# Optimization experiments

Measured on AMD Instinct MI355X. Metric: run time of the kernel, lower is better.

The kernel has to match this reference:

```python
import jax, jax.numpy as jnp
import numpy as np

N = 200000
H = W = 1024
C_IN, C_MID = 256, 64
EPS = 1e-6


def _build_neighbor_idx():
    # Sample N unique occupied sites on an HxW grid; build 3x3 kernel maps.
    rng = np.random.default_rng(0)
    perm = rng.permutation(H * W)[:N]
    grid = -np.ones(H * W, dtype=np.int64)
    grid[perm] = np.arange(N)
    ys, xs = perm // W, perm % W
    maps = []
    for dy in (-1, 0, 1):
        for dx in (-1, 0, 1):
            ny, nx = ys + dy, xs + dx
            valid = (ny >= 0) & (ny < H) & (nx >= 0) & (nx < W)
            lin = np.clip(ny * W + nx, 0, H * W - 1)
            nb = grid[lin]
            maps.append(np.where(valid & (nb >= 0), nb, N))  # sentinel N = missing
    return jnp.asarray(np.stack(maps).astype(np.int32))  # [9, N]


def setup_inputs() -> dict:
    key = jax.random.key(0)
    ks = jax.random.split(key, 4)
    return {
        "x": jax.random.normal(ks[0], (N, C_IN), jnp.float32),
        "W1": jax.random.normal(ks[1], (C_IN, C_MID), jnp.float32) * (C_IN ** -0.5),
        "W2": jax.random.normal(ks[2], (9, C_MID, C_MID), jnp.float32) * ((9 * C_MID) ** -0.5),
        "W3": jax.random.normal(ks[3], (C_MID, C_IN), jnp.float32) * (C_MID ** -0.5),
        "g1": jnp.ones((C_MID,), jnp.float32),
        "b1": jnp.zeros((C_MID,), jnp.float32),
        "g2": jnp.ones((C_MID,), jnp.float32),
        "b2": jnp.zeros((C_MID,), jnp.float32),
        "g3": jnp.ones((C_IN,), jnp.float32),
        "b3": jnp.zeros((C_IN,), jnp.float32),
        "neighbor_idx": _build_neighbor_idx(),
    }


def _ln(h, g, b):
    mu = jnp.mean(h, axis=-1, keepdims=True)
    var = jnp.mean(jnp.square(h - mu), axis=-1, keepdims=True)
    return (h - mu) * jax.lax.rsqrt(var + EPS) * g + b


def reference(x, W1, W2, W3, g1, b1, g2, b2, g3, b3, neighbor_idx):
    # conv1 (1x1 sparse conv == per-point linear) -> LN -> GELU
    h = jax.nn.gelu(_ln(x @ W1, g1, b1), approximate=False)
    # conv2: 3x3 sparse conv via gather-GEMM over kernel maps, sentinel row = zeros
    h_pad = jnp.concatenate([h, jnp.zeros((1, h.shape[1]), h.dtype)], axis=0)
    gathered = h_pad[neighbor_idx]               # [9, N, C_MID]
    h = jnp.einsum('knc,kcd->nd', gathered, W2)  # [N, C_MID]
    h = jax.nn.gelu(_ln(h, g2, b2), approximate=False)
    # conv3 (1x1) -> LN, residual, GELU
    h = _ln(h @ W3, g3, b3)
    return jax.nn.gelu(h + x, approximate=False)
```

## Files before the change

kernel.cpp:

```cpp
#include <hip/hip_runtime.h>
#include <math.h>

#define NPTS 200000
#define LNEPS 1e-6f

typedef unsigned short u16;
typedef __attribute__((ext_vector_type(4))) float  f4;
typedef __attribute__((ext_vector_type(8))) short  s8;

__device__ __forceinline__ u16 f2b(float f) {
    union { float f; unsigned u; } v; v.f = f;
    unsigned r = v.u + 0x7fffu + ((v.u >> 16) & 1u);
    return (u16)(r >> 16);
}

__device__ __forceinline__ float gelu_f(float v) {
    float u = v * (0.7978845608028654f + 0.035677408136300125f * v * v);
    u = fminf(u, 15.0f);
    float e = __builtin_amdgcn_exp2f(u * 2.8853900817779268f);
    return 0.5f * v * (1.0f + (e - 1.0f) * __builtin_amdgcn_rcpf(e + 1.0f));
}

__global__ __launch_bounds__(256) void k0_convw(
    const float* __restrict__ W1, const float* __restrict__ W2,
    const float* __restrict__ W3,
    u16* __restrict__ W1f, u16* __restrict__ W2f, u16* __restrict__ W3f,
    u16* __restrict__ h1)
{
    int t = blockIdx.x * 256 + threadIdx.x;
    if (t < 16384) {
        int j = t & 7, l = (t >> 3) & 63, ks = (t >> 9) & 7, nt = t >> 12;
        int k = 32 * ks + (l >> 4) * 8 + j;
        int n = 16 * nt + (l & 15);
        W1f[t] = f2b(W1[k * 64 + n]);
    }
    if (t < 36864) {
        int kk = t >> 12;
        int r = t & 4095;
        int j = r & 7, l = (r >> 3) & 63, ks = (r >> 9) & 1, nt = r >> 10;
        int k = 32 * ks + (l >> 4) * 8 + j;
        int n = 16 * nt + (l & 15);
        W2f[t] = f2b(W2[(kk * 64 + k) * 64 + n]);
    }
    if (t < 16384) {
        int j = t & 7, l = (t >> 3) & 63, ks = (t >> 9) & 1, nt = t >> 10;
        int k = 32 * ks + (l >> 4) * 8 + j;
        int n = 16 * nt + (l & 15);
        W3f[t] = f2b(W3[k * 256 + n]);
    }
    if (t < 64) h1[(long)NPTS * 64 + t] = 0;
}

__global__ __launch_bounds__(256) void k1_conv1(
    const float* __restrict__ x, const u16* __restrict__ W1f,
    const float* __restrict__ g1, const float* __restrict__ b1,
    u16* __restrict__ h1)
{
    int tid = threadIdx.x;
    int w = tid >> 6, l = tid & 63, lg = l >> 4, lr = l & 15;
    long base = (long)blockIdx.x * 64 + w * 16;
    const float* xrow = x + (base + lr) * 256;

    f4 xa[16];
    #pragma unroll
    for (int ks = 0; ks < 8; ++ks) {
        xa[2 * ks]     = *(const f4*)(xrow + 32 * ks + lg * 8);
        xa[2 * ks + 1] = *(const f4*)(xrow + 32 * ks + lg * 8 + 4);
    }

    f4 acc[4] = {};
    #pragma unroll
    for (int ks = 0; ks < 8; ++ks) {
        f4 a0 = xa[2 * ks], a1 = xa[2 * ks + 1];
        s8 a;
        a[0] = (short)f2b(a0[0]); a[1] = (short)f2b(a0[1]);
        a[2] = (short)f2b(a0[2]); a[3] = (short)f2b(a0[3]);
        a[4] = (short)f2b(a1[0]); a[5] = (short)f2b(a1[1]);
        a[6] = (short)f2b(a1[2]); a[7] = (short)f2b(a1[3]);
        #pragma unroll
        for (int nt = 0; nt < 4; ++nt) {
            s8 b = *(const s8*)(W1f + ((nt * 8 + ks) * 64 + l) * 8);
            acc[nt] = __builtin_amdgcn_mfma_f32_16x16x32_bf16(a, b, acc[nt], 0, 0, 0);
        }
    }

    #pragma unroll
    for (int r = 0; r < 4; ++r) {
        float sv = 0.f, qv = 0.f;
        #pragma unroll
        for (int nt = 0; nt < 4; ++nt) { float v = acc[nt][r]; sv += v; qv += v * v; }
        #pragma unroll
        for (int m = 1; m < 16; m <<= 1) { sv += __shfl_xor(sv, m); qv += __shfl_xor(qv, m); }
        float mu  = sv * (1.0f / 64.0f);
        float var = qv * (1.0f / 64.0f) - mu * mu;
        float rs  = rsqrtf(var + LNEPS);
        long row = base + lg * 4 + r;
        #pragma unroll
        for (int nt = 0; nt < 4; ++nt) {
            int col = 16 * nt + lr;
            float v = (acc[nt][r] - mu) * rs * g1[col] + b1[col];
            h1[row * 64 + col] = f2b(gelu_f(v));
        }
    }
}

__global__ __launch_bounds__(256, 4) void k2a_conv2(
    const u16* __restrict__ h1, const u16* __restrict__ W2f,
    const float* __restrict__ g2, const float* __restrict__ b2,
    const int* __restrict__ nidx, u16* __restrict__ h2)
{
    int tid = threadIdx.x;
    int w = tid >> 6, l = tid & 63, lg = l >> 4, lr = l & 15;
    long base = (long)blockIdx.x * 64 + w * 16;
    long rowa = base + lr;

    int idxs[9];
    #pragma unroll
    for (int k = 0; k < 9; ++k) idxs[k] = nidx[(long)k * NPTS + rowa];

    s8 afr[9][2];
    #pragma unroll
    for (int k = 0; k < 9; ++k) {
        const u16* arow = h1 + (long)idxs[k] * 64;
        afr[k][0] = *(const s8*)(arow + lg * 8);
        afr[k][1] = *(const s8*)(arow + 32 + lg * 8);
    }

    f4 acc2[4] = {};
    #pragma unroll
    for (int k = 0; k < 9; ++k) {
        #pragma unroll
        for (int ks = 0; ks < 2; ++ks) {
            #pragma unroll
            for (int nt = 0; nt < 4; ++nt) {
                s8 b = *(const s8*)(W2f + (long)k * 4096 + ((nt * 2 + ks) * 64 + l) * 8);
                acc2[nt] = __builtin_amdgcn_mfma_f32_16x16x32_bf16(afr[k][ks], b, acc2[nt], 0, 0, 0);
            }
        }
    }

    #pragma unroll
    for (int r = 0; r < 4; ++r) {
        float sv = 0.f, qv = 0.f;
        #pragma unroll
        for (int nt = 0; nt < 4; ++nt) { float v = acc2[nt][r]; sv += v; qv += v * v; }
        #pragma unroll
        for (int m = 1; m < 16; m <<= 1) { sv += __shfl_xor(sv, m); qv += __shfl_xor(qv, m); }
        float mu  = sv * (1.0f / 64.0f);
        float var = qv * (1.0f / 64.0f) - mu * mu;
        float rs  = rsqrtf(var + LNEPS);
        long row = base + lg * 4 + r;
        #pragma unroll
        for (int nt = 0; nt < 4; ++nt) {
            int col = 16 * nt + lr;
            float v = (acc2[nt][r] - mu) * rs * g2[col] + b2[col];
            h2[row * 64 + col] = f2b(gelu_f(v));
        }
    }
}

__global__ __launch_bounds__(256, 4) void k2b_conv3(
    const u16* __restrict__ h2, const u16* __restrict__ W3f,
    const float* __restrict__ x,
    const float* __restrict__ g3, const float* __restrict__ b3,
    float* __restrict__ out)
{
    int tid = threadIdx.x;
    int w = tid >> 6, l = tid & 63, lg = l >> 4, lr = l & 15;
    long base = (long)blockIdx.x * 64 + w * 16;

    const u16* arow = h2 + (base + lr) * 64;
    s8 a0 = *(const s8*)(arow + lg * 8);
    s8 a1 = *(const s8*)(arow + 32 + lg * 8);

    f4 acc3[16] = {};
    #pragma unroll
    for (int nt = 0; nt < 16; ++nt) {
        s8 b0 = *(const s8*)(W3f + ((nt * 2 + 0) * 64 + l) * 8);
        s8 b1 = *(const s8*)(W3f + ((nt * 2 + 1) * 64 + l) * 8);
        acc3[nt] = __builtin_amdgcn_mfma_f32_16x16x32_bf16(a0, b0, acc3[nt], 0, 0, 0);
        acc3[nt] = __builtin_amdgcn_mfma_f32_16x16x32_bf16(a1, b1, acc3[nt], 0, 0, 0);
    }

    #pragma unroll
    for (int r = 0; r < 4; ++r) {
        float sv = 0.f, qv = 0.f;
        #pragma unroll
        for (int nt = 0; nt < 16; ++nt) { float v = acc3[nt][r]; sv += v; qv += v * v; }
        #pragma unroll
        for (int m = 1; m < 16; m <<= 1) { sv += __shfl_xor(sv, m); qv += __shfl_xor(qv, m); }
        float mu  = sv * (1.0f / 256.0f);
        float var = qv * (1.0f / 256.0f) - mu * mu;
        float rs  = rsqrtf(var + LNEPS);
        long row = base + lg * 4 + r;
        const float* xr = x + row * 256;
        float* outr = out + row * 256;
        #pragma unroll
        for (int nt = 0; nt < 16; ++nt) {
            int col = 16 * nt + lr;
            float v = (acc3[nt][r] - mu) * rs * g3[col] + b3[col];
            v += xr[col];
            outr[col] = gelu_f(v);
        }
    }
}

extern "C" void kernel_launch(void* const* d_in, const int* in_sizes, int n_in,
                              void* d_out, int out_size, void* d_ws, size_t ws_size,
                              hipStream_t stream)
{
    const float* x  = (const float*)d_in[0];
    const float* W1 = (const float*)d_in[1];
    const float* W2 = (const float*)d_in[2];
    const float* W3 = (const float*)d_in[3];
    const float* g1 = (const float*)d_in[4];
    const float* b1 = (const float*)d_in[5];
    const float* g2 = (const float*)d_in[6];
    const float* b2 = (const float*)d_in[7];
    const float* g3 = (const float*)d_in[8];
    const float* b3 = (const float*)d_in[9];
    const int* nidx = (const int*)d_in[10];
    float* out = (float*)d_out;

    char* ws = (char*)d_ws;
    u16* W1f = (u16*)(ws);
    u16* W2f = (u16*)(ws + 32768);
    u16* W3f = (u16*)(ws + 106496);
    u16* h1  = (u16*)(ws + 139264);
    u16* h2  = (u16*)(ws + 139264 + 25600128);

    hipLaunchKernelGGL(k0_convw, dim3(144), dim3(256), 0, stream,
                       W1, W2, W3, W1f, W2f, W3f, h1);
    hipLaunchKernelGGL(k1_conv1, dim3(3125), dim3(256), 0, stream,
                       x, W1f, g1, b1, h1);
    hipLaunchKernelGGL(k2a_conv2, dim3(3125), dim3(256), 0, stream,
                       h1, W2f, g2, b2, nidx, h2);
    hipLaunchKernelGGL(k2b_conv3, dim3(3125), dim3(256), 0, stream,
                       h2, W3f, x, g3, b3, out);
}
```

Baseline: 220.2 us.

## Stage conv1 input and conv3 epilogue through LDS for coalesced access

conv1 now loads the fp32 x tile cooperatively with coalesced 16-byte loads, converts it to bf16 once and stores it in a swizzled LDS tile. The MFMA A-fragments are then read from LDS. conv3 writes the normalized outputs to an LDS staging buffer so the residual read of x and the output store become row-contiguous float4 accesses instead of scattered scalar ones. This adds LDS usage and block barriers, and lowers the occupancy hint for conv3.

```diff
diff --git a/kernel.cpp b/kernel.cpp
--- a/kernel.cpp
+++ b/kernel.cpp
@@ -7,6 +7,7 @@
 typedef unsigned short u16;
 typedef __attribute__((ext_vector_type(4))) float  f4;
 typedef __attribute__((ext_vector_type(8))) short  s8;
+typedef __attribute__((ext_vector_type(4))) short  s4;
 
 __device__ __forceinline__ u16 f2b(float f) {
     union { float f; unsigned u; } v; v.f = f;
@@ -56,27 +57,32 @@
     const float* __restrict__ g1, const float* __restrict__ b1,
     u16* __restrict__ h1)
 {
+    __shared__ __align__(16) u16 xt[64][256];
     int tid = threadIdx.x;
+    long base = (long)blockIdx.x * 64;
+
+    #pragma unroll
+    for (int p = 0; p < 16; ++p) {
+        int row  = p * 4 + (tid >> 6);
+        int col4 = (tid & 63) * 4;
+        f4 v = *(const f4*)(x + (base + row) * 256 + col4);
+        s4 bv;
+        bv[0] = (short)f2b(v[0]); bv[1] = (short)f2b(v[1]);
+        bv[2] = (short)f2b(v[2]); bv[3] = (short)f2b(v[3]);
+        int byte = (col4 * 2) ^ ((row & 7) << 4);
+        *(s4*)((char*)&xt[row][0] + byte) = bv;
+    }
+    __syncthreads();
+
     int w = tid >> 6, l = tid & 63, lg = l >> 4, lr = l & 15;
-    long base = (long)blockIdx.x * 64 + w * 16;
-    const float* xrow = x + (base + lr) * 256;
-
-    f4 xa[16];
+    int arow = w * 16 + lr;
+    long mbase = base + w * 16;
+
+    f4 acc[4] = {};
     #pragma unroll
     for (int ks = 0; ks < 8; ++ks) {
-        xa[2 * ks]     = *(const f4*)(xrow + 32 * ks + lg * 8);
-        xa[2 * ks + 1] = *(const f4*)(xrow + 32 * ks + lg * 8 + 4);
-    }
-
-    f4 acc[4] = {};
-    #pragma unroll
-    for (int ks = 0; ks < 8; ++ks) {
-        f4 a0 = xa[2 * ks], a1 = xa[2 * ks + 1];
-        s8 a;
-        a[0] = (short)f2b(a0[0]); a[1] = (short)f2b(a0[1]);
-        a[2] = (short)f2b(a0[2]); a[3] = (short)f2b(a0[3]);
-        a[4] = (short)f2b(a1[0]); a[5] = (short)f2b(a1[1]);
-        a[6] = (short)f2b(a1[2]); a[7] = (short)f2b(a1[3]);
+        int byte = ((ks * 64 + lg * 16)) ^ ((arow & 7) << 4);
+        s8 a = *(const s8*)((const char*)&xt[arow][0] + byte);
         #pragma unroll
         for (int nt = 0; nt < 4; ++nt) {
             s8 b = *(const s8*)(W1f + ((nt * 8 + ks) * 64 + l) * 8);
@@ -94,7 +100,7 @@
         float mu  = sv * (1.0f / 64.0f);
         float var = qv * (1.0f / 64.0f) - mu * mu;
         float rs  = rsqrtf(var + LNEPS);
-        long row = base + lg * 4 + r;
+        long row = mbase + lg * 4 + r;
         #pragma unroll
         for (int nt = 0; nt < 4; ++nt) {
             int col = 16 * nt + lr;
@@ -159,12 +165,13 @@
     }
 }
 
-__global__ __launch_bounds__(256, 4) void k2b_conv3(
+__global__ __launch_bounds__(256, 3) void k2b_conv3(
     const u16* __restrict__ h2, const u16* __restrict__ W3f,
     const float* __restrict__ x,
     const float* __restrict__ g3, const float* __restrict__ b3,
     float* __restrict__ out)
 {
+    __shared__ __align__(16) float ot[4][4][264];
     int tid = threadIdx.x;
     int w = tid >> 6, l = tid & 63, lg = l >> 4, lr = l & 15;
     long base = (long)blockIdx.x * 64 + w * 16;
@@ -192,16 +199,33 @@
         float mu  = sv * (1.0f / 256.0f);
         float var = qv * (1.0f / 256.0f) - mu * mu;
         float rs  = rsqrtf(var + LNEPS);
-        long row = base + lg * 4 + r;
-        const float* xr = x + row * 256;
-        float* outr = out + row * 256;
+
         #pragma unroll
         for (int nt = 0; nt < 16; ++nt) {
             int col = 16 * nt + lr;
-            float v = (acc3[nt][r] - mu) * rs * g3[col] + b3[col];
-            v += xr[col];
-            outr[col] = gelu_f(v);
-        }
+            ot[w][lg][col] = (acc3[nt][r] - mu) * rs * g3[col] + b3[col];
+        }
+        __syncthreads();
+
+        int rsel = l >> 4;
+        long gr = base - lr  + 0;
+        gr = (long)blockIdx.x * 64 + w * 16 + rsel * 4 + r;
+        const float* xr = x + gr * 256;
+        float* outr = out + gr * 256;
+        int c0 = (l & 15) * 4;
+        #pragma unroll
+        for (int c = 0; c < 4; ++c) {
+            int col = c0 + 64 * c;
+            f4 lv = *(const f4*)&ot[w][rsel][col];
+            f4 xv = *(const f4*)(xr + col);
+            f4 ov;
+            ov[0] = gelu_f(lv[0] + xv[0]);
+            ov[1] = gelu_f(lv[1] + xv[1]);
+            ov[2] = gelu_f(lv[2] + xv[2]);
+            ov[3] = gelu_f(lv[3] + xv[3]);
+            *(f4*)(outr + col) = ov;
+        }
+        __syncthreads();
     }
 }
 
```

Result: no change. 221.2 us (+0.5%).
